# Kernel tuning notes

Hardware: AMD Instinct MI355X
Metric: run time of the kernel (lower is better)

## Reference

```python
import jax, jax.numpy as jnp
import numpy as np

# Grid constants from init_kwargs: output_shape = [1, 10, 200, 176, 64]
D, H, W, C = 10, 200, 176, 64
N_VOX = 30000


def _conv_block(x, w, scale, bias, stride, pad):
    # x: [N,C,D,H,W]; w: [O,I,kd,kh,kw]; ZeroPad3d then valid Conv3d,
    # then fused (inference) BatchNorm3d + ReLU.
    x = jnp.pad(x, ((0, 0), (0, 0), (pad[0], pad[0]), (pad[1], pad[1]), (pad[2], pad[2])))
    x = jax.lax.conv_general_dilated(
        x, w, window_strides=stride, padding='VALID',
        dimension_numbers=('NCDHW', 'OIDHW', 'NCDHW'))
    s = scale[None, :, None, None, None]
    b = bias[None, :, None, None, None]
    return jax.nn.relu(x * s + b)


def setup_inputs() -> dict:
    key = jax.random.key(0)
    kf, kd, kh, kw, k1, k2, k3, ks = jax.random.split(key, 8)
    voxel_features = jax.random.normal(kf, (N_VOX, C), dtype=jnp.float32)
    # coors columns: (batch_idx, d, h, w) each in range
    b_idx = jnp.zeros((N_VOX,), dtype=jnp.int32)  # batch_size = 1
    d_idx = jax.random.randint(kd, (N_VOX,), 0, D, dtype=jnp.int32)
    h_idx = jax.random.randint(kh, (N_VOX,), 0, H, dtype=jnp.int32)
    w_idx = jax.random.randint(kw, (N_VOX,), 0, W, dtype=jnp.int32)
    coors = jnp.stack([b_idx, d_idx, h_idx, w_idx], axis=1)
    fan = 1.0 / np.sqrt(C * 27)
    W1 = jax.random.normal(k1, (64, C, 3, 3, 3), dtype=jnp.float32) * fan
    W2 = jax.random.normal(k2, (64, 64, 3, 3, 3), dtype=jnp.float32) * fan
    W3 = jax.random.normal(k3, (64, 64, 3, 3, 3), dtype=jnp.float32) * fan
    ks1, ks2, ks3 = jax.random.split(ks, 3)
    scale1 = jax.random.uniform(ks1, (64,), dtype=jnp.float32, minval=0.5, maxval=1.5)
    scale2 = jax.random.uniform(ks2, (64,), dtype=jnp.float32, minval=0.5, maxval=1.5)
    scale3 = jax.random.uniform(ks3, (64,), dtype=jnp.float32, minval=0.5, maxval=1.5)
    bias1 = jax.random.normal(jax.random.fold_in(ks1, 1), (64,), dtype=jnp.float32) * 0.1
    bias2 = jax.random.normal(jax.random.fold_in(ks2, 1), (64,), dtype=jnp.float32) * 0.1
    bias3 = jax.random.normal(jax.random.fold_in(ks3, 1), (64,), dtype=jnp.float32) * 0.1
    return {
        'voxel_features': voxel_features, 'coors': coors, 'batch_size': 1,
        'W1': W1, 'scale1': scale1, 'bias1': bias1,
        'W2': W2, 'scale2': scale2, 'bias2': bias2,
        'W3': W3, 'scale3': scale3, 'bias3': bias3,
    }


def reference(voxel_features, coors, batch_size,
              W1, scale1, bias1, W2, scale2, bias2, W3, scale3, bias3):
    # scatter_nd: sparse voxel features -> dense [B, D, H, W, C]
    dense = jnp.zeros((batch_size, D, H, W, C), dtype=voxel_features.dtype)
    dense = dense.at[coors[:, 0], coors[:, 1], coors[:, 2], coors[:, 3]].set(voxel_features)
    x = dense.transpose(0, 4, 1, 2, 3)  # [B, C, D, H, W]
    # middle_conv: Pad(1)+Conv3d s=(2,1,1); Pad(0,1,1)+Conv3d s=1; Pad(1)+Conv3d s=(2,1,1)
    x = _conv_block(x, W1, scale1, bias1, (2, 1, 1), (1, 1, 1))   # D: 10 -> 5
    x = _conv_block(x, W2, scale2, bias2, (1, 1, 1), (0, 1, 1))   # D: 5 -> 3
    x = _conv_block(x, W3, scale3, bias3, (2, 1, 1), (1, 1, 1))   # D: 3 -> 2
    N, Cc, Dd, Hh, Ww = x.shape
    return x.reshape(N, Cc * Dd, Hh, Ww)  # [B, 128, H, W]
```

## Files before the change

### kernel.cpp

```cpp
#include <hip/hip_runtime.h>
#include <cstddef>

#define HH 200
#define WW 176
#define HP 202
#define WP 178
#define D_IN 10
#define D1 5
#define D2 3
#define D3 2
#define SLICE ((size_t)HP * WP * 64)

#define LDSA_ROW 3200
#define LDSB_OFF 32256
#define LDS_BYTES 138240

typedef _Float16 h8 __attribute__((ext_vector_type(8)));
typedef float f4 __attribute__((ext_vector_type(4)));

__device__ __forceinline__ void gl_lds16(const void* g, void* l) {
    __builtin_amdgcn_global_load_lds(
        (const __attribute__((address_space(1))) void*)g,
        (__attribute__((address_space(3))) void*)l, 16, 0, 0);
}

__global__ __launch_bounds__(256) void wtrans_k(const float* __restrict__ src,
                                                _Float16* __restrict__ dst) {
    int idx = blockIdx.x * 256 + threadIdx.x;
    if (idx >= 27 * 64 * 64) return;
    int ci = idx & 63;
    int co = (idx >> 6) & 63;
    int tap = idx >> 12;
    int s = ci >> 3, j = ci & 7;
    dst[tap * 4096 + co * 64 + (((s ^ (co & 7)) << 3) | j)] =
        (_Float16)src[(co * 64 + ci) * 27 + tap];
}

__global__ __launch_bounds__(256) void winner_k(const int* __restrict__ coors,
                                                int* __restrict__ winner, int nvox) {
    int v = blockIdx.x * 256 + threadIdx.x;
    if (v >= nvox) return;
    int d = coors[v * 4 + 1], h = coors[v * 4 + 2], w = coors[v * 4 + 3];
    atomicMax(&winner[(d * HH + h) * WW + w], v + 1);
}

__global__ __launch_bounds__(256) void scatter_k(const float* __restrict__ feat,
                                                 const int* __restrict__ coors,
                                                 const int* __restrict__ winner,
                                                 _Float16* __restrict__ A, int nvox) {
    int v = blockIdx.x * 4 + (threadIdx.x >> 6);
    int ci = threadIdx.x & 63;
    if (v >= nvox) return;
    int d = coors[v * 4 + 1], h = coors[v * 4 + 2], w = coors[v * 4 + 3];
    if (winner[(d * HH + h) * WW + w] != v + 1) return;
    int P = w + 1;
    int swz = (((ci >> 3) ^ (P & 7)) << 3) | (ci & 7);
    A[(size_t)d * SLICE + ((size_t)(h + 1) * WP + P) * 64 + swz] = (_Float16)feat[v * 64 + ci];
}

__global__ __launch_bounds__(256) void halo_k(_Float16* __restrict__ A2,
                                              _Float16* __restrict__ A3) {
    const int s = blockIdx.x;
    _Float16* base = (s < D1) ? (A2 + (size_t)s * SLICE) : (A3 + (size_t)(s - D1) * SLICE);
    const h8 z = {};
    for (int t = threadIdx.x; t < 6080; t += 256) {
        size_t off;
        if (t < 2848) {
            int r = t / 1424, c = t - r * 1424;
            off = (size_t)(r ? (HP - 1) : 0) * WP * 64 + (size_t)c * 8;
        } else {
            int u = t - 2848;
            int c = u / 1616, v = u - c * 1616;
            int hr = v >> 3, o = v & 7;
            off = ((size_t)hr * WP + (c ? (WP - 1) : 0)) * 64 + (size_t)o * 8;
        }
        *(h8*)(base + off) = z;
    }
}

template <int FINAL>
__global__ __launch_bounds__(512, 2) void conv_mfma_k(
    const _Float16* __restrict__ in, void* __restrict__ outp,
    const _Float16* __restrict__ wt,
    const float* __restrict__ scale, const float* __restrict__ bias,
    int inD, int strideD, int padD) {
    extern __shared__ char smem_raw[];
    _Float16* smem = (_Float16*)smem_raw;

    const int lane = threadIdx.x & 63;
    const int wave = threadIdx.x >> 6;
    const int l16 = lane & 15;
    const int quad = lane >> 4;
    const int h0 = blockIdx.y * 8;
    const int wb = blockIdx.x * 48;
    const int d = blockIdx.z;

    f4 acc[3][4];
#pragma unroll
    for (int mt = 0; mt < 3; ++mt)
#pragma unroll
        for (int nt = 0; nt < 4; ++nt) acc[mt][nt] = (f4){0.f, 0.f, 0.f, 0.f};

    for (int kd = 0; kd < 3; ++kd) {
        const int zd = d * strideD + kd - padD;
        if (zd < 0 || zd >= inD) continue;
        const _Float16* __restrict__ aplane = in + (size_t)zd * SLICE;
        const _Float16* __restrict__ wkd = wt + (size_t)kd * 9 * 4096;

        __syncthreads();
        for (int j = wave; j < 135; j += 8) {
            if (j < 63) {
                int c = j * 64 + lane;
                int r = c / 400;
                int rem = c - r * 400;
                if (r > 9) r = 9;
                int px = rem >> 3, s = rem & 7;
                int g = wb + px;
                if (g > 177) g = 177;
                gl_lds16(aplane + ((size_t)(h0 + r) * WP + g) * 64 + s * 8,
                         smem_raw + j * 1024);
            } else {
                int c = (j - 63) * 64 + lane;
                gl_lds16(wkd + c * 8, smem_raw + 64512 + (j - 63) * 1024);
            }
        }
        __syncthreads();

#pragma unroll
        for (int kh = 0; kh < 3; ++kh) {
#pragma unroll
            for (int kw = 0; kw < 3; ++kw) {
#pragma unroll
                for (int ch = 0; ch < 2; ++ch) {
                    const int q = ch * 4 + quad;
                    const int tap = kh * 3 + kw;
                    h8 b[4];
#pragma unroll
                    for (int nt = 0; nt < 4; ++nt)
                        b[nt] = *(const h8*)(smem + LDSB_OFF + tap * 4096 +
                                             (nt * 16 + l16) * 64 + ((q ^ (l16 & 7)) << 3));
#pragma unroll
                    for (int mt = 0; mt < 3; ++mt) {
                        const int px = mt * 16 + l16 + kw;
                        h8 a = *(const h8*)(smem + (wave + kh) * LDSA_ROW +
                                            px * 64 + ((q ^ (px & 7)) << 3));
#pragma unroll
                        for (int nt = 0; nt < 4; ++nt)
                            acc[mt][nt] = __builtin_amdgcn_mfma_f32_16x16x32_f16(
                                a, b[nt], acc[mt][nt], 0, 0, 0);
                    }
                }
            }
        }
    }

    const int h = h0 + wave;
#pragma unroll
    for (int nt = 0; nt < 4; ++nt) {
        const int co = nt * 16 + l16;
        const float s = scale[co];
        const float bb = bias[co];
#pragma unroll
        for (int mt = 0; mt < 3; ++mt) {
            const int w0 = wb + mt * 16 + quad * 4;
            if (w0 < WW) {
                if (FINAL) {
                    f4 v;
#pragma unroll
                    for (int r = 0; r < 4; ++r) {
                        float x = acc[mt][nt][r] * s + bb;
                        v[r] = x > 0.f ? x : 0.f;
                    }
                    *(f4*)((float*)outp + (((size_t)(co * 2 + d)) * HH + h) * WW + w0) = v;
                } else {
#pragma unroll
                    for (int r = 0; r < 4; ++r) {
                        float x = acc[mt][nt][r] * s + bb;
                        x = x > 0.f ? x : 0.f;
                        const int P = w0 + r + 1;
                        const int swz = (((co >> 3) ^ (P & 7)) << 3) | (co & 7);
                        ((_Float16*)outp)[(size_t)d * SLICE +
                            ((size_t)(h + 1) * WP + P) * 64 + swz] = (_Float16)x;
                    }
                }
            }
        }
    }
}

extern "C" void kernel_launch(void* const* d_in, const int* in_sizes, int n_in,
                              void* d_out, int out_size, void* d_ws, size_t ws_size,
                              hipStream_t stream) {
    const float* feat   = (const float*)d_in[0];
    const int*   coors  = (const int*)d_in[1];
    const float* W1     = (const float*)d_in[3];
    const float* scale1 = (const float*)d_in[4];
    const float* bias1  = (const float*)d_in[5];
    const float* W2     = (const float*)d_in[6];
    const float* scale2 = (const float*)d_in[7];
    const float* bias2  = (const float*)d_in[8];
    const float* W3     = (const float*)d_in[9];
    const float* scale3 = (const float*)d_in[10];
    const float* bias3  = (const float*)d_in[11];
    const int nvox = in_sizes[0] / 64;

    const size_t nA1 = (size_t)D_IN * SLICE;
    const size_t nWin = (size_t)D_IN * HH * WW;
    const size_t nA2 = (size_t)D1 * SLICE;
    const size_t nA3 = (size_t)D2 * SLICE;
    const size_t nWT = (size_t)27 * 64 * 64;

    _Float16* A1 = (_Float16*)d_ws;
    int* win = (int*)(A1 + nA1);
    _Float16* A2 = (_Float16*)(win + nWin);
    _Float16* A3 = A2 + nA2;
    _Float16* wt1 = A3 + nA3;
    _Float16* wt2 = wt1 + nWT;
    _Float16* wt3 = wt2 + nWT;

    hipFuncSetAttribute((const void*)conv_mfma_k<0>,
                        hipFuncAttributeMaxDynamicSharedMemorySize, LDS_BYTES);
    hipFuncSetAttribute((const void*)conv_mfma_k<1>,
                        hipFuncAttributeMaxDynamicSharedMemorySize, LDS_BYTES);

    hipMemsetAsync(d_ws, 0, nA1 * sizeof(_Float16) + nWin * sizeof(int), stream);
    halo_k<<<dim3(D1 + D2), 256, 0, stream>>>(A2, A3);

    const int nwt_blk = (27 * 64 * 64 + 255) / 256;
    wtrans_k<<<nwt_blk, 256, 0, stream>>>(W1, wt1);
    wtrans_k<<<nwt_blk, 256, 0, stream>>>(W2, wt2);
    wtrans_k<<<nwt_blk, 256, 0, stream>>>(W3, wt3);

    winner_k<<<(nvox + 255) / 256, 256, 0, stream>>>(coors, win, nvox);
    scatter_k<<<(nvox + 3) / 4, 256, 0, stream>>>(feat, coors, win, A1, nvox);

    dim3 blk(512);
    conv_mfma_k<0><<<dim3(4, 25, D1), blk, LDS_BYTES, stream>>>(A1, A2, wt1, scale1, bias1, D_IN, 2, 1);
    conv_mfma_k<0><<<dim3(4, 25, D2), blk, LDS_BYTES, stream>>>(A2, A3, wt2, scale2, bias2, D1, 1, 0);
    conv_mfma_k<1><<<dim3(4, 25, D3), blk, LDS_BYTES, stream>>>(A3, (float*)d_out, wt3, scale3, bias3, D2, 2, 1);
}
```

Baseline: 219.4 us.

## Shrink conv tiles to 4 rows and stage weights per kh row in LDS

The conv kernel now uses 256-thread blocks covering 4 output rows instead of 8, which doubles the grid. Weights are staged one kh row (3 taps) at a time rather than all 9 taps, so LDS use drops from about 135KB to about 62KB and more blocks can be resident per CU. The cost is more barriers and repeated weight loads per block, plus extra halo row reloading. The three weight-transpose launches are also merged into one.

```diff
diff --git a/kernel.cpp b/kernel.cpp
--- a/kernel.cpp
+++ b/kernel.cpp
@@ -11,9 +11,8 @@
 #define D3 2
 #define SLICE ((size_t)HP * WP * 64)
 
-#define LDSA_ROW 3200
-#define LDSB_OFF 32256
-#define LDS_BYTES 138240
+#define LB_OFF 38912
+#define LDS_TOTAL (38912 + 24576)
 
 typedef _Float16 h8 __attribute__((ext_vector_type(8)));
 typedef float f4 __attribute__((ext_vector_type(4)));
@@ -24,15 +23,20 @@
         (__attribute__((address_space(3))) void*)l, 16, 0, 0);
 }
 
-__global__ __launch_bounds__(256) void wtrans_k(const float* __restrict__ src,
+__global__ __launch_bounds__(256) void wtrans_k(const float* __restrict__ W1,
+                                                const float* __restrict__ W2,
+                                                const float* __restrict__ W3,
                                                 _Float16* __restrict__ dst) {
     int idx = blockIdx.x * 256 + threadIdx.x;
-    if (idx >= 27 * 64 * 64) return;
-    int ci = idx & 63;
-    int co = (idx >> 6) & 63;
-    int tap = idx >> 12;
+    if (idx >= 3 * 27 * 64 * 64) return;
+    int set = idx / (27 * 64 * 64);
+    int r = idx - set * (27 * 64 * 64);
+    const float* src = set == 0 ? W1 : (set == 1 ? W2 : W3);
+    int ci = r & 63;
+    int co = (r >> 6) & 63;
+    int tap = r >> 12;
     int s = ci >> 3, j = ci & 7;
-    dst[tap * 4096 + co * 64 + (((s ^ (co & 7)) << 3) | j)] =
+    dst[set * 110592 + tap * 4096 + co * 64 + (((s ^ (co & 7)) << 3) | j)] =
         (_Float16)src[(co * 64 + ci) * 27 + tap];
 }
 
@@ -79,19 +83,19 @@
 }
 
 template <int FINAL>
-__global__ __launch_bounds__(512, 2) void conv_mfma_k(
+__global__ __launch_bounds__(256, 2) void conv_mfma_k(
     const _Float16* __restrict__ in, void* __restrict__ outp,
     const _Float16* __restrict__ wt,
     const float* __restrict__ scale, const float* __restrict__ bias,
     int inD, int strideD, int padD) {
-    extern __shared__ char smem_raw[];
+    __shared__ char smem_raw[LDS_TOTAL];
     _Float16* smem = (_Float16*)smem_raw;
 
     const int lane = threadIdx.x & 63;
     const int wave = threadIdx.x >> 6;
     const int l16 = lane & 15;
     const int quad = lane >> 4;
-    const int h0 = blockIdx.y * 8;
+    const int h0 = blockIdx.y * 4;
     const int wb = blockIdx.x * 48;
     const int d = blockIdx.z;
 
@@ -105,44 +109,43 @@
         const int zd = d * strideD + kd - padD;
         if (zd < 0 || zd >= inD) continue;
         const _Float16* __restrict__ aplane = in + (size_t)zd * SLICE;
-        const _Float16* __restrict__ wkd = wt + (size_t)kd * 9 * 4096;
-
-        __syncthreads();
-        for (int j = wave; j < 135; j += 8) {
-            if (j < 63) {
-                int c = j * 64 + lane;
-                int r = c / 400;
-                int rem = c - r * 400;
-                if (r > 9) r = 9;
-                int px = rem >> 3, s = rem & 7;
-                int g = wb + px;
-                if (g > 177) g = 177;
-                gl_lds16(aplane + ((size_t)(h0 + r) * WP + g) * 64 + s * 8,
-                         smem_raw + j * 1024);
-            } else {
-                int c = (j - 63) * 64 + lane;
-                gl_lds16(wkd + c * 8, smem_raw + 64512 + (j - 63) * 1024);
-            }
-        }
-        __syncthreads();
-
-#pragma unroll
+
         for (int kh = 0; kh < 3; ++kh) {
+            __syncthreads();
+            if (kh == 0) {
+                for (int j = wave; j < 38; j += 4) {
+                    int c = j * 64 + lane;
+                    int r = c / 400;
+                    int rem = c - r * 400;
+                    if (r > 5) { r = 5; rem = c - 2000; }
+                    int px = rem >> 3, s = rem & 7;
+                    int g = wb + px;
+                    if (g > 177) g = 177;
+                    gl_lds16(aplane + ((size_t)(h0 + r) * WP + g) * 64 + s * 8,
+                             smem_raw + j * 1024);
+                }
+            }
+            {
+                const _Float16* __restrict__ wrow = wt + (size_t)(kd * 9 + kh * 3) * 4096;
+                for (int j = wave; j < 24; j += 4)
+                    gl_lds16(wrow + (j * 64 + lane) * 8, smem_raw + LB_OFF + j * 1024);
+            }
+            __syncthreads();
+
 #pragma unroll
             for (int kw = 0; kw < 3; ++kw) {
 #pragma unroll
                 for (int ch = 0; ch < 2; ++ch) {
                     const int q = ch * 4 + quad;
-                    const int tap = kh * 3 + kw;
                     h8 b[4];
 #pragma unroll
                     for (int nt = 0; nt < 4; ++nt)
-                        b[nt] = *(const h8*)(smem + LDSB_OFF + tap * 4096 +
-                                             (nt * 16 + l16) * 64 + ((q ^ (l16 & 7)) << 3));
+                        b[nt] = *(const h8*)(smem + (LB_OFF / 2) + (kw * 64 + nt * 16 + l16) * 64 +
+                                             ((q ^ (l16 & 7)) << 3));
 #pragma unroll
                     for (int mt = 0; mt < 3; ++mt) {
                         const int px = mt * 16 + l16 + kw;
-                        h8 a = *(const h8*)(smem + (wave + kh) * LDSA_ROW +
+                        h8 a = *(const h8*)(smem + (wave + kh) * 3200 +
                                             px * 64 + ((q ^ (px & 7)) << 3));
 #pragma unroll
                         for (int nt = 0; nt < 4; ++nt)
@@ -218,24 +221,17 @@
     _Float16* wt2 = wt1 + nWT;
     _Float16* wt3 = wt2 + nWT;
 
-    hipFuncSetAttribute((const void*)conv_mfma_k<0>,
-                        hipFuncAttributeMaxDynamicSharedMemorySize, LDS_BYTES);
-    hipFuncSetAttribute((const void*)conv_mfma_k<1>,
-                        hipFuncAttributeMaxDynamicSharedMemorySize, LDS_BYTES);
-
     hipMemsetAsync(d_ws, 0, nA1 * sizeof(_Float16) + nWin * sizeof(int), stream);
     halo_k<<<dim3(D1 + D2), 256, 0, stream>>>(A2, A3);
 
-    const int nwt_blk = (27 * 64 * 64 + 255) / 256;
-    wtrans_k<<<nwt_blk, 256, 0, stream>>>(W1, wt1);
-    wtrans_k<<<nwt_blk, 256, 0, stream>>>(W2, wt2);
-    wtrans_k<<<nwt_blk, 256, 0, stream>>>(W3, wt3);
+    const int nwt_blk = (3 * 27 * 64 * 64 + 255) / 256;
+    wtrans_k<<<nwt_blk, 256, 0, stream>>>(W1, W2, W3, wt1);
 
     winner_k<<<(nvox + 255) / 256, 256, 0, stream>>>(coors, win, nvox);
     scatter_k<<<(nvox + 3) / 4, 256, 0, stream>>>(feat, coors, win, A1, nvox);
 
-    dim3 blk(512);
-    conv_mfma_k<0><<<dim3(4, 25, D1), blk, LDS_BYTES, stream>>>(A1, A2, wt1, scale1, bias1, D_IN, 2, 1);
-    conv_mfma_k<0><<<dim3(4, 25, D2), blk, LDS_BYTES, stream>>>(A2, A3, wt2, scale2, bias2, D1, 1, 0);
-    conv_mfma_k<1><<<dim3(4, 25, D3), blk, LDS_BYTES, stream>>>(A3, (float*)d_out, wt3, scale3, bias3, D2, 2, 1);
-}
+    dim3 blk(256);
+    conv_mfma_k<0><<<dim3(4, 50, D1), blk, 0, stream>>>(A1, A2, wt1, scale1, bias1, D_IN, 2, 1);
+    conv_mfma_k<0><<<dim3(4, 50, D2), blk, 0, stream>>>(A2, A3, wt2, scale2, bias2, D1, 1, 0);
+    conv_mfma_k<1><<<dim3(4, 50, D3), blk, 0, stream>>>(A3, (float*)d_out, wt3, scale3, bias3, D2, 2, 1);
+}
```

New measurement: 206.1 us. -6.1%, faster.
